# Kernel optimization log

Hardware: AMD Instinct MI355X
Metric: run time of the kernel (lower is better)

Reference implementation:

```python
import jax, jax.numpy as jnp
from jax import lax
import numpy as np
import math

INPUT_DIM = 64
HIDDEN_DIM = 512
SEQ_LEN = 256
BATCH = 512
PRED_LEN = 24
NUM_TARGETS = 1


def setup_inputs() -> dict:
    key = jax.random.key(0)
    ks = jax.random.split(key, 10)
    stdv = 1.0 / math.sqrt(HIDDEN_DIM)
    u = lambda k, shape: jax.random.uniform(k, shape, jnp.float32, -stdv, stdv)
    return {
        "x": jax.random.normal(ks[0], (BATCH, SEQ_LEN, INPUT_DIM), jnp.float32),
        "Wa": u(ks[1], (INPUT_DIM, INPUT_DIM)),
        "Ua": u(ks[2], (2 * HIDDEN_DIM, INPUT_DIM)),
        "ba": jnp.zeros((INPUT_DIM,), jnp.float32),
        "Va": u(ks[3], (INPUT_DIM, INPUT_DIM)),
        "W_ih": u(ks[4], (4 * HIDDEN_DIM, INPUT_DIM)),
        "W_hh": u(ks[5], (4 * HIDDEN_DIM, HIDDEN_DIM)),
        "b_ih": u(ks[6], (4 * HIDDEN_DIM,)),
        "b_hh": u(ks[7], (4 * HIDDEN_DIM,)),
        "fc_w": u(ks[8], (PRED_LEN * NUM_TARGETS, HIDDEN_DIM)),
        "fc_b": u(ks[9], (PRED_LEN * NUM_TARGETS,)),
    }


def reference(x, Wa, Ua, ba, Va, W_ih, W_hh, b_ih, b_hh, fc_w, fc_b):
    B, S, D = x.shape
    H = W_hh.shape[1]

    def step(carry, x_t):
        h, c = carry  # [B,H] each
        # attention gate over input features
        hc = jnp.concatenate([h, c], axis=1)  # [B,2H]
        a_t = jnp.tanh(x_t @ Wa + hc @ Ua + ba) @ Va  # [B,D]
        alpha_t = jax.nn.softmax(a_t, axis=1)
        x_att = alpha_t * x_t
        # torch.nn.LSTMCell: gates in order i, f, g, o
        gates = x_att @ W_ih.T + h @ W_hh.T + b_ih + b_hh  # [B,4H]
        i, f, g, o = jnp.split(gates, 4, axis=1)
        c_new = jax.nn.sigmoid(f) * c + jax.nn.sigmoid(i) * jnp.tanh(g)
        h_new = jax.nn.sigmoid(o) * jnp.tanh(c_new)
        return (h_new, c_new), None

    h0 = jnp.zeros((B, H), x.dtype)
    c0 = jnp.zeros((B, H), x.dtype)
    (h_T, _), _ = lax.scan(step, (h0, c0), jnp.swapaxes(x, 0, 1))  # scan over seq
    y = h_T @ fc_w.T + fc_b  # [B, pred_len*num_targets]
    return y.reshape(B, PRED_LEN, NUM_TARGETS)
```

## Files before the change

kernel.cpp:

```cpp
#include <hip/hip_runtime.h>
#include <math.h>

#define B 512
#define S 256
#define D 64
#define H 512
#define BH (B*H)


typedef __attribute__((ext_vector_type(8))) short short8;
typedef __attribute__((ext_vector_type(4))) float f32x4;

__device__ inline unsigned short f2bf(float v) {
    unsigned int u = __float_as_uint(v);
    unsigned int r = (u + 0x7fffu + ((u >> 16) & 1u)) >> 16;
    return (unsigned short)r;
}
__device__ inline float bf2f(unsigned short b) {
    return __uint_as_float(((unsigned int)b) << 16);
}

__global__ __launch_bounds__(256) void init_zero(
    float* __restrict__ h32, float* __restrict__ c32,
    unsigned short* __restrict__ hHi, unsigned short* __restrict__ hLo)
{
    int i = blockIdx.x * blockDim.x + threadIdx.x;
    if (i < BH) {
        h32[i] = 0.f;
        c32[i] = 0.f;
        hHi[i] = 0;
        hLo[i] = 0;
    }
}

__global__ __launch_bounds__(256) void prep_weights(
    const float* __restrict__ Whh, const float* __restrict__ Wih,
    unsigned short* __restrict__ wswz)
{
    const int ut = blockIdx.x;
    const int kb = blockIdx.y;
    const int t = threadIdx.x;
    const int srow = t >> 2;
    const int cc0 = (t & 3) * 16;
    const int Wrow = (srow & 3)*H + ut*16 + (srow >> 2);

    const float* src = (kb < 8) ? (Whh + (size_t)Wrow*H + kb*64 + cc0)
                                : (Wih + (size_t)Wrow*D + cc0);
    float v[16];
    #pragma unroll
    for (int i = 0; i < 4; ++i)
        *(float4*)&v[i*4] = *(const float4*)(src + i*4);

    unsigned short hi[16], lo[16];
    #pragma unroll
    for (int e = 0; e < 16; ++e) {
        hi[e] = f2bf(v[e]);
        lo[e] = f2bf(v[e] - bf2f(hi[e]));
    }
    #pragma unroll
    for (int g = 0; g < 2; ++g) {
        const int cc = cc0 + g*8;
        const int ks = cc >> 5;
        const int cg = (cc >> 3) & 3;
        size_t bh = ((((size_t)(ut*9 + kb)*2 + 0)*2 + ks)*64 + srow)*32 + cg*8;
        size_t bl = ((((size_t)(ut*9 + kb)*2 + 1)*2 + ks)*64 + srow)*32 + cg*8;
        *(short8*)(wswz + bh) = *(const short8*)&hi[g*8];
        *(short8*)(wswz + bl) = *(const short8*)&lo[g*8];
    }
}

__global__ __launch_bounds__(256) void attn_kernel(
    const float* __restrict__ x, const float* __restrict__ Wa,
    const float* __restrict__ Ua, const float* __restrict__ ba,
    const float* __restrict__ Va,
    const float* __restrict__ h32, const float* __restrict__ c32,
    unsigned short* __restrict__ xHi, unsigned short* __restrict__ xLo, int t)
{
    const int d = threadIdx.x & 63;
    const int r = (threadIdx.x >> 6) & 1;
    const int p = threadIdx.x >> 7;
    const int b = blockIdx.x * 2 + r;

    const int rd = t & 1;
    const float* __restrict__ hrow = h32 + (size_t)rd*BH + (size_t)b*H;
    const float* __restrict__ crow = c32 + (size_t)b*H;
    const float* __restrict__ xrow = x + ((size_t)b*S + t)*D;

    __shared__ float part[2][2][64];
    __shared__ float ta[2][64];
    __shared__ float pv[2][2][64];

    float a = 0.f;
    if (p == 0) {
        a = ba[d];
        #pragma unroll 8
        for (int k = 0; k < D; ++k) a += xrow[k] * Wa[k*D + d];
        #pragma unroll 8
        for (int k = 0; k < H; ++k) a += hrow[k] * Ua[k*D + d];
    } else {
        #pragma unroll 8
        for (int k = 0; k < H; ++k) a += crow[k] * Ua[(size_t)(H + k)*D + d];
    }
    part[r][p][d] = a;
    __syncthreads();
    if (p == 0) {
        ta[r][d] = tanhf(part[r][0][d] + part[r][1][d]);
    }
    __syncthreads();
    float av = 0.f;
    {
        const int k0 = p * 32;
        #pragma unroll 8
        for (int k = k0; k < k0 + 32; ++k) av += ta[r][k] * Va[k*D + d];
    }
    pv[r][p][d] = av;
    __syncthreads();
    float v = pv[r][0][d] + pv[r][1][d];
    float m = v;
    #pragma unroll
    for (int o = 32; o > 0; o >>= 1) m = fmaxf(m, __shfl_xor(m, o));
    float e = expf(v - m);
    float ssum = e;
    #pragma unroll
    for (int o = 32; o > 0; o >>= 1) ssum += __shfl_xor(ssum, o);
    if (p == 0) {
        float val = (e / ssum) * xrow[d];
        unsigned short hi = f2bf(val);
        unsigned short lo = f2bf(val - bf2f(hi));
        xHi[(size_t)b*D + d] = hi;
        xLo[(size_t)b*D + d] = lo;
    }
}

__global__ __launch_bounds__(256) void gates_kernel(
    const unsigned short* __restrict__ wswz,
    const unsigned short* __restrict__ hHi, const unsigned short* __restrict__ hLo,
    const unsigned short* __restrict__ xHi, const unsigned short* __restrict__ xLo,
    float* __restrict__ h32, float* __restrict__ c32,
    const float* __restrict__ bih, const float* __restrict__ bhh, int t)
{
    const int tid = threadIdx.x;
    const int lane = tid & 63;
    const int wid = tid >> 6;
    const int wr = wid >> 1, wc = wid & 1;
    const int ut = blockIdx.x;
    const int rt = blockIdx.y;
    const int b0 = rt * 64;
    const int u_base = ut * 16;
    const int l15 = lane & 15;
    const int cg = lane >> 4;

    __shared__ __align__(16) unsigned short aHi[2][64][72];
    __shared__ __align__(16) unsigned short aLo[2][64][72];
    __shared__ float gout[64][66];

    const int rd = t & 1, wrs = rd ^ 1;
    const unsigned short* __restrict__ hHiR = hHi + (size_t)rd*BH;
    const unsigned short* __restrict__ hLoR = hLo + (size_t)rd*BH;

    f32x4 acc00 = {0,0,0,0}, acc01 = {0,0,0,0}, acc10 = {0,0,0,0}, acc11 = {0,0,0,0};
    short8 bre[2][2][2][2];

    const int srow = tid >> 2;
    const int q4 = tid & 3;

    auto stageA = [&](int kb, int buf) {
        const unsigned short *sh, *sl;
        if (kb < 8) {
            size_t base = (size_t)(b0 + srow)*H + kb*64 + q4*16;
            sh = hHiR + base; sl = hLoR + base;
        } else {
            size_t base = (size_t)(b0 + srow)*D + q4*16;
            sh = xHi + base; sl = xLo + base;
        }
        *(short8*)&aHi[buf][srow][q4*16]     = *(const short8*)sh;
        *(short8*)&aHi[buf][srow][q4*16 + 8] = *(const short8*)(sh + 8);
        *(short8*)&aLo[buf][srow][q4*16]     = *(const short8*)sl;
        *(short8*)&aLo[buf][srow][q4*16 + 8] = *(const short8*)(sl + 8);
    };
    auto loadB = [&](int kb, int set) {
        #pragma unroll
        for (int half = 0; half < 2; ++half)
            #pragma unroll
            for (int ks = 0; ks < 2; ++ks)
                #pragma unroll
                for (int rb = 0; rb < 2; ++rb) {
                    const unsigned short* p = wswz +
                        ((((size_t)(ut*9 + kb)*2 + half)*2 + ks)*64
                         + wc*32 + rb*16 + l15)*32 + cg*8;
                    bre[set][half][ks][rb] = *(const short8*)p;
                }
    };

    stageA(0, 0);
    loadB(0, 0);
    __syncthreads();

    #pragma unroll
    for (int kb = 0; kb < 9; ++kb) {
        const int cur = kb & 1;
        if (kb < 8) {
            stageA(kb + 1, cur ^ 1);
            loadB(kb + 1, cur ^ 1);
        }
        #pragma unroll
        for (int ks = 0; ks < 2; ++ks) {
            const int col = ks*32 + cg*8;
            short8 ah0 = *(const short8*)&aHi[cur][wr*32 + l15][col];
            short8 ah1 = *(const short8*)&aHi[cur][wr*32 + 16 + l15][col];
            short8 al0 = *(const short8*)&aLo[cur][wr*32 + l15][col];
            short8 al1 = *(const short8*)&aLo[cur][wr*32 + 16 + l15][col];
            short8 bh0 = bre[cur][0][ks][0];
            short8 bh1 = bre[cur][0][ks][1];
            short8 bl0 = bre[cur][1][ks][0];
            short8 bl1 = bre[cur][1][ks][1];
            acc00 = __builtin_amdgcn_mfma_f32_16x16x32_bf16(ah0, bh0, acc00, 0,0,0);
            acc01 = __builtin_amdgcn_mfma_f32_16x16x32_bf16(ah0, bh1, acc01, 0,0,0);
            acc10 = __builtin_amdgcn_mfma_f32_16x16x32_bf16(ah1, bh0, acc10, 0,0,0);
            acc11 = __builtin_amdgcn_mfma_f32_16x16x32_bf16(ah1, bh1, acc11, 0,0,0);
            acc00 = __builtin_amdgcn_mfma_f32_16x16x32_bf16(ah0, bl0, acc00, 0,0,0);
            acc01 = __builtin_amdgcn_mfma_f32_16x16x32_bf16(ah0, bl1, acc01, 0,0,0);
            acc10 = __builtin_amdgcn_mfma_f32_16x16x32_bf16(ah1, bl0, acc10, 0,0,0);
            acc11 = __builtin_amdgcn_mfma_f32_16x16x32_bf16(ah1, bl1, acc11, 0,0,0);
            acc00 = __builtin_amdgcn_mfma_f32_16x16x32_bf16(al0, bh0, acc00, 0,0,0);
            acc01 = __builtin_amdgcn_mfma_f32_16x16x32_bf16(al0, bh1, acc01, 0,0,0);
            acc10 = __builtin_amdgcn_mfma_f32_16x16x32_bf16(al1, bh0, acc10, 0,0,0);
            acc11 = __builtin_amdgcn_mfma_f32_16x16x32_bf16(al1, bh1, acc11, 0,0,0);
        }
        __syncthreads();
    }

    {
        const int m0 = (lane >> 4) * 4;
        const int n0 = lane & 15;
        #pragma unroll
        for (int r = 0; r < 4; ++r) {
            gout[wr*32 + m0 + r     ][wc*32 + n0     ] = acc00[r];
            gout[wr*32 + m0 + r     ][wc*32 + 16 + n0] = acc01[r];
            gout[wr*32 + 16 + m0 + r][wc*32 + n0     ] = acc10[r];
            gout[wr*32 + 16 + m0 + r][wc*32 + 16 + n0] = acc11[r];
        }
    }
    __syncthreads();
    {
        const int u16 = tid & 15;
        const int u_glob = u_base + u16;
        const float bs0 = bih[0*H + u_glob] + bhh[0*H + u_glob];
        const float bs1 = bih[1*H + u_glob] + bhh[1*H + u_glob];
        const float bs2 = bih[2*H + u_glob] + bhh[2*H + u_glob];
        const float bs3 = bih[3*H + u_glob] + bhh[3*H + u_glob];
        float* __restrict__ h32w = h32 + (size_t)wrs*BH;
        unsigned short* __restrict__ hHiW = (unsigned short*)hHi + (size_t)wrs*BH;
        unsigned short* __restrict__ hLoW = (unsigned short*)hLo + (size_t)wrs*BH;
        #pragma unroll
        for (int pass = 0; pass < 4; ++pass) {
            const int b_loc = (tid >> 4) + pass*16;
            const int b = b0 + b_loc;
            float2 g01 = *(const float2*)&gout[b_loc][u16*4];
            float2 g23 = *(const float2*)&gout[b_loc][u16*4 + 2];
            float gi = g01.x + bs0;
            float gf = g01.y + bs1;
            float gg = g23.x + bs2;
            float go = g23.y + bs3;
            const size_t idx = (size_t)b*H + u_glob;
            float c_old = c32[idx];
            float si = 1.f/(1.f + expf(-gi));
            float sf = 1.f/(1.f + expf(-gf));
            float so = 1.f/(1.f + expf(-go));
            float cn = sf*c_old + si*tanhf(gg);
            float hn = so*tanhf(cn);
            c32[idx] = cn;
            h32w[idx] = hn;
            unsigned short hi = f2bf(hn);
            unsigned short lo = f2bf(hn - bf2f(hi));
            hHiW[idx] = hi;
            hLoW[idx] = lo;
        }
    }
}

__global__ __launch_bounds__(256) void fc_kernel(
    const float* __restrict__ fcw, const float* __restrict__ fcb,
    const float* __restrict__ h32, float* __restrict__ out)
{
    const int b = blockIdx.x;
    __shared__ float hrow[H];
    const float* __restrict__ hp = h32 + (size_t)b*H;
    for (int k = threadIdx.x; k < H; k += 256) hrow[k] = hp[k];
    __syncthreads();
    int j = threadIdx.x;
    if (j < 24) {
        float a = fcb[j];
        #pragma unroll 8
        for (int k = 0; k < H; ++k) a += hrow[k] * fcw[j*H + k];
        out[b*24 + j] = a;
    }
}

extern "C" void kernel_launch(void* const* d_in, const int* in_sizes, int n_in,
                              void* d_out, int out_size, void* d_ws, size_t ws_size,
                              hipStream_t stream) {
    const float* x   = (const float*)d_in[0];
    const float* Wa  = (const float*)d_in[1];
    const float* Ua  = (const float*)d_in[2];
    const float* ba  = (const float*)d_in[3];
    const float* Va  = (const float*)d_in[4];
    const float* Wih = (const float*)d_in[5];
    const float* Whh = (const float*)d_in[6];
    const float* bih = (const float*)d_in[7];
    const float* bhh = (const float*)d_in[8];
    const float* fcw = (const float*)d_in[9];
    const float* fcb = (const float*)d_in[10];
    float* out = (float*)d_out;

    char* base = (char*)d_ws;
    float* h32 = (float*)(base);
    float* c32 = (float*)(base + (size_t)2*BH*4);
    unsigned short* hHi = (unsigned short*)(base + (size_t)3*BH*4);
    unsigned short* hLo = hHi + (size_t)2*BH;
    unsigned short* xHi = hLo + (size_t)2*BH;
    unsigned short* xLo = xHi + (size_t)B*D;
    unsigned short* wswz = xLo + (size_t)B*D;

    hipLaunchKernelGGL(init_zero, dim3((BH + 255)/256), dim3(256), 0, stream,
                       h32, c32, hHi, hLo);
    hipLaunchKernelGGL(prep_weights, dim3(32, 9), dim3(256), 0, stream,
                       Whh, Wih, wswz);
    for (int t = 0; t < S; ++t) {
        hipLaunchKernelGGL(attn_kernel, dim3(B/2), dim3(256), 0, stream,
                           x, Wa, Ua, ba, Va, h32, c32, xHi, xLo, t);
        hipLaunchKernelGGL(gates_kernel, dim3(32, 8), dim3(256), 0, stream,
                           wswz, hHi, hLo, xHi, xLo, h32, c32, bih, bhh, t);
    }
    hipLaunchKernelGGL(fc_kernel, dim3(B), dim3(256), 0, stream, fcw, fcb, h32, out);
}
```

Baseline: 8.384 ms.

## Halve gate-column tile per block to double grid size in gates kernel

The gates kernel now covers 8 hidden units (32 gate columns) per block instead of 16, so the grid grows from 256 to 512 blocks on the 256-CU device. The weight swizzle layout is rebuilt to match, B fragments are loaded directly per k-block instead of being double-buffered in registers, and launch bounds request 2 blocks per CU. This aims to fill more CUs on a latency-bound per-timestep GEMM. In exchange, each A tile of h is now staged from global memory by twice as many blocks, and weight loads are no longer prefetched.

```diff
diff --git a/kernel.cpp b/kernel.cpp
--- a/kernel.cpp
+++ b/kernel.cpp
@@ -6,7 +6,6 @@
 #define D 64
 #define H 512
 #define BH (B*H)
-
 
 typedef __attribute__((ext_vector_type(8))) short short8;
 typedef __attribute__((ext_vector_type(4))) float f32x4;
@@ -37,36 +36,33 @@
     const float* __restrict__ Whh, const float* __restrict__ Wih,
     unsigned short* __restrict__ wswz)
 {
-    const int ut = blockIdx.x;
+    const int jt = blockIdx.x;
     const int kb = blockIdx.y;
     const int t = threadIdx.x;
-    const int srow = t >> 2;
-    const int cc0 = (t & 3) * 16;
-    const int Wrow = (srow & 3)*H + ut*16 + (srow >> 2);
-
-    const float* src = (kb < 8) ? (Whh + (size_t)Wrow*H + kb*64 + cc0)
-                                : (Wih + (size_t)Wrow*D + cc0);
-    float v[16];
+    const int jj = t >> 3;
+    const int kk8 = t & 7;
+    const int jg = jt*32 + jj;
+    const int u = jg >> 2, q = jg & 3;
+    const int Wrow = q*H + u;
+
+    const float* src = (kb < 8) ? (Whh + (size_t)Wrow*H + kb*64 + kk8*8)
+                                : (Wih + (size_t)Wrow*D + kk8*8);
+    float v[8];
+    *(float4*)&v[0] = *(const float4*)(src);
+    *(float4*)&v[4] = *(const float4*)(src + 4);
+
+    unsigned short hi[8], lo[8];
     #pragma unroll
-    for (int i = 0; i < 4; ++i)
-        *(float4*)&v[i*4] = *(const float4*)(src + i*4);
-
-    unsigned short hi[16], lo[16];
-    #pragma unroll
-    for (int e = 0; e < 16; ++e) {
+    for (int e = 0; e < 8; ++e) {
         hi[e] = f2bf(v[e]);
         lo[e] = f2bf(v[e] - bf2f(hi[e]));
     }
-    #pragma unroll
-    for (int g = 0; g < 2; ++g) {
-        const int cc = cc0 + g*8;
-        const int ks = cc >> 5;
-        const int cg = (cc >> 3) & 3;
-        size_t bh = ((((size_t)(ut*9 + kb)*2 + 0)*2 + ks)*64 + srow)*32 + cg*8;
-        size_t bl = ((((size_t)(ut*9 + kb)*2 + 1)*2 + ks)*64 + srow)*32 + cg*8;
-        *(short8*)(wswz + bh) = *(const short8*)&hi[g*8];
-        *(short8*)(wswz + bl) = *(const short8*)&lo[g*8];
-    }
+    const int ks = kk8 >> 2, cg = kk8 & 3;
+    const size_t slab = (size_t)(jt*9 + kb) * 4096;
+    const size_t oH = slab + (size_t)(0*2048 + ks*1024 + cg*256 + jj*8);
+    const size_t oL = slab + (size_t)(1*2048 + ks*1024 + cg*256 + jj*8);
+    *(short8*)(wswz + oH) = *(const short8*)hi;
+    *(short8*)(wswz + oL) = *(const short8*)lo;
 }
 
 __global__ __launch_bounds__(256) void attn_kernel(
@@ -132,7 +128,7 @@
     }
 }
 
-__global__ __launch_bounds__(256) void gates_kernel(
+__global__ __launch_bounds__(256, 2) void gates_kernel(
     const unsigned short* __restrict__ wswz,
     const unsigned short* __restrict__ hHi, const unsigned short* __restrict__ hLo,
     const unsigned short* __restrict__ xHi, const unsigned short* __restrict__ xLo,
@@ -143,108 +139,92 @@
     const int lane = tid & 63;
     const int wid = tid >> 6;
     const int wr = wid >> 1, wc = wid & 1;
-    const int ut = blockIdx.x;
-    const int rt = blockIdx.y;
-    const int b0 = rt * 64;
-    const int u_base = ut * 16;
+    const int jt = blockIdx.x;
+    const int b0 = blockIdx.y * 64;
     const int l15 = lane & 15;
     const int cg = lane >> 4;
 
     __shared__ __align__(16) unsigned short aHi[2][64][72];
     __shared__ __align__(16) unsigned short aLo[2][64][72];
-    __shared__ float gout[64][66];
+    __shared__ float gout[64][37];
 
     const int rd = t & 1, wrs = rd ^ 1;
     const unsigned short* __restrict__ hHiR = hHi + (size_t)rd*BH;
     const unsigned short* __restrict__ hLoR = hLo + (size_t)rd*BH;
 
-    f32x4 acc00 = {0,0,0,0}, acc01 = {0,0,0,0}, acc10 = {0,0,0,0}, acc11 = {0,0,0,0};
-    short8 bre[2][2][2][2];
-
     const int srow = tid >> 2;
     const int q4 = tid & 3;
 
-    auto stageA = [&](int kb, int buf) {
-        const unsigned short *sh, *sl;
-        if (kb < 8) {
-            size_t base = (size_t)(b0 + srow)*H + kb*64 + q4*16;
-            sh = hHiR + base; sl = hLoR + base;
-        } else {
-            size_t base = (size_t)(b0 + srow)*D + q4*16;
-            sh = xHi + base; sl = xLo + base;
-        }
-        *(short8*)&aHi[buf][srow][q4*16]     = *(const short8*)sh;
-        *(short8*)&aHi[buf][srow][q4*16 + 8] = *(const short8*)(sh + 8);
-        *(short8*)&aLo[buf][srow][q4*16]     = *(const short8*)sl;
-        *(short8*)&aLo[buf][srow][q4*16 + 8] = *(const short8*)(sl + 8);
-    };
-    auto loadB = [&](int kb, int set) {
-        #pragma unroll
-        for (int half = 0; half < 2; ++half)
-            #pragma unroll
-            for (int ks = 0; ks < 2; ++ks)
-                #pragma unroll
-                for (int rb = 0; rb < 2; ++rb) {
-                    const unsigned short* p = wswz +
-                        ((((size_t)(ut*9 + kb)*2 + half)*2 + ks)*64
-                         + wc*32 + rb*16 + l15)*32 + cg*8;
-                    bre[set][half][ks][rb] = *(const short8*)p;
-                }
-    };
-
-    stageA(0, 0);
-    loadB(0, 0);
-    __syncthreads();
-
-    #pragma unroll
+    {
+        const size_t base = (size_t)(b0 + srow)*H + q4*16;
+        *(short8*)&aHi[0][srow][q4*16]     = *(const short8*)(hHiR + base);
+        *(short8*)&aHi[0][srow][q4*16 + 8] = *(const short8*)(hHiR + base + 8);
+        *(short8*)&aLo[0][srow][q4*16]     = *(const short8*)(hLoR + base);
+        *(short8*)&aLo[0][srow][q4*16 + 8] = *(const short8*)(hLoR + base + 8);
+    }
+    __syncthreads();
+
+    f32x4 acc0 = {0,0,0,0}, acc1 = {0,0,0,0};
+    const int lofs = cg*256 + (wc*16 + l15)*8;
+
     for (int kb = 0; kb < 9; ++kb) {
         const int cur = kb & 1;
+        const unsigned short* pB = wswz + (size_t)(jt*9 + kb)*4096;
+        short8 bh0 = *(const short8*)(pB + 0*2048 + 0*1024 + lofs);
+        short8 bh1 = *(const short8*)(pB + 0*2048 + 1*1024 + lofs);
+        short8 bl0 = *(const short8*)(pB + 1*2048 + 0*1024 + lofs);
+        short8 bl1 = *(const short8*)(pB + 1*2048 + 1*1024 + lofs);
         if (kb < 8) {
-            stageA(kb + 1, cur ^ 1);
-            loadB(kb + 1, cur ^ 1);
+            const unsigned short *sh, *sl;
+            if (kb + 1 < 8) {
+                const size_t base = (size_t)(b0 + srow)*H + (kb + 1)*64 + q4*16;
+                sh = hHiR + base; sl = hLoR + base;
+            } else {
+                const size_t base = (size_t)(b0 + srow)*D + q4*16;
+                sh = xHi + base; sl = xLo + base;
+            }
+            *(short8*)&aHi[cur^1][srow][q4*16]     = *(const short8*)sh;
+            *(short8*)&aHi[cur^1][srow][q4*16 + 8] = *(const short8*)(sh + 8);
+            *(short8*)&aLo[cur^1][srow][q4*16]     = *(const short8*)sl;
+            *(short8*)&aLo[cur^1][srow][q4*16 + 8] = *(const short8*)(sl + 8);
         }
-        #pragma unroll
-        for (int ks = 0; ks < 2; ++ks) {
-            const int col = ks*32 + cg*8;
-            short8 ah0 = *(const short8*)&aHi[cur][wr*32 + l15][col];
-            short8 ah1 = *(const short8*)&aHi[cur][wr*32 + 16 + l15][col];
-            short8 al0 = *(const short8*)&aLo[cur][wr*32 + l15][col];
-            short8 al1 = *(const short8*)&aLo[cur][wr*32 + 16 + l15][col];
-            short8 bh0 = bre[cur][0][ks][0];
-            short8 bh1 = bre[cur][0][ks][1];
-            short8 bl0 = bre[cur][1][ks][0];
-            short8 bl1 = bre[cur][1][ks][1];
-            acc00 = __builtin_amdgcn_mfma_f32_16x16x32_bf16(ah0, bh0, acc00, 0,0,0);
-            acc01 = __builtin_amdgcn_mfma_f32_16x16x32_bf16(ah0, bh1, acc01, 0,0,0);
-            acc10 = __builtin_amdgcn_mfma_f32_16x16x32_bf16(ah1, bh0, acc10, 0,0,0);
-            acc11 = __builtin_amdgcn_mfma_f32_16x16x32_bf16(ah1, bh1, acc11, 0,0,0);
-            acc00 = __builtin_amdgcn_mfma_f32_16x16x32_bf16(ah0, bl0, acc00, 0,0,0);
-            acc01 = __builtin_amdgcn_mfma_f32_16x16x32_bf16(ah0, bl1, acc01, 0,0,0);
-            acc10 = __builtin_amdgcn_mfma_f32_16x16x32_bf16(ah1, bl0, acc10, 0,0,0);
-            acc11 = __builtin_amdgcn_mfma_f32_16x16x32_bf16(ah1, bl1, acc11, 0,0,0);
-            acc00 = __builtin_amdgcn_mfma_f32_16x16x32_bf16(al0, bh0, acc00, 0,0,0);
-            acc01 = __builtin_amdgcn_mfma_f32_16x16x32_bf16(al0, bh1, acc01, 0,0,0);
-            acc10 = __builtin_amdgcn_mfma_f32_16x16x32_bf16(al1, bh0, acc10, 0,0,0);
-            acc11 = __builtin_amdgcn_mfma_f32_16x16x32_bf16(al1, bh1, acc11, 0,0,0);
-        }
+        const int ar = wr*32 + l15;
+        short8 ah00 = *(const short8*)&aHi[cur][ar     ][cg*8];
+        short8 ah01 = *(const short8*)&aHi[cur][ar     ][32 + cg*8];
+        short8 ah10 = *(const short8*)&aHi[cur][ar + 16][cg*8];
+        short8 ah11 = *(const short8*)&aHi[cur][ar + 16][32 + cg*8];
+        short8 al00 = *(const short8*)&aLo[cur][ar     ][cg*8];
+        short8 al01 = *(const short8*)&aLo[cur][ar     ][32 + cg*8];
+        short8 al10 = *(const short8*)&aLo[cur][ar + 16][cg*8];
+        short8 al11 = *(const short8*)&aLo[cur][ar + 16][32 + cg*8];
+
+        acc0 = __builtin_amdgcn_mfma_f32_16x16x32_bf16(ah00, bh0, acc0, 0,0,0);
+        acc1 = __builtin_amdgcn_mfma_f32_16x16x32_bf16(ah10, bh0, acc1, 0,0,0);
+        acc0 = __builtin_amdgcn_mfma_f32_16x16x32_bf16(ah00, bl0, acc0, 0,0,0);
+        acc1 = __builtin_amdgcn_mfma_f32_16x16x32_bf16(ah10, bl0, acc1, 0,0,0);
+        acc0 = __builtin_amdgcn_mfma_f32_16x16x32_bf16(al00, bh0, acc0, 0,0,0);
+        acc1 = __builtin_amdgcn_mfma_f32_16x16x32_bf16(al10, bh0, acc1, 0,0,0);
+        acc0 = __builtin_amdgcn_mfma_f32_16x16x32_bf16(ah01, bh1, acc0, 0,0,0);
+        acc1 = __builtin_amdgcn_mfma_f32_16x16x32_bf16(ah11, bh1, acc1, 0,0,0);
+        acc0 = __builtin_amdgcn_mfma_f32_16x16x32_bf16(ah01, bl1, acc0, 0,0,0);
+        acc1 = __builtin_amdgcn_mfma_f32_16x16x32_bf16(ah11, bl1, acc1, 0,0,0);
+        acc0 = __builtin_amdgcn_mfma_f32_16x16x32_bf16(al01, bh1, acc0, 0,0,0);
+        acc1 = __builtin_amdgcn_mfma_f32_16x16x32_bf16(al11, bh1, acc1, 0,0,0);
         __syncthreads();
     }
 
     {
-        const int m0 = (lane >> 4) * 4;
-        const int n0 = lane & 15;
+        const int m0 = cg * 4;
         #pragma unroll
         for (int r = 0; r < 4; ++r) {
-            gout[wr*32 + m0 + r     ][wc*32 + n0     ] = acc00[r];
-            gout[wr*32 + m0 + r     ][wc*32 + 16 + n0] = acc01[r];
-            gout[wr*32 + 16 + m0 + r][wc*32 + n0     ] = acc10[r];
-            gout[wr*32 + 16 + m0 + r][wc*32 + 16 + n0] = acc11[r];
+            gout[wr*32 + m0 + r     ][wc*16 + l15] = acc0[r];
+            gout[wr*32 + 16 + m0 + r][wc*16 + l15] = acc1[r];
         }
     }
     __syncthreads();
     {
-        const int u16 = tid & 15;
-        const int u_glob = u_base + u16;
+        const int u8 = tid & 7;
+        const int u_glob = jt*8 + u8;
         const float bs0 = bih[0*H + u_glob] + bhh[0*H + u_glob];
         const float bs1 = bih[1*H + u_glob] + bhh[1*H + u_glob];
         const float bs2 = bih[2*H + u_glob] + bhh[2*H + u_glob];
@@ -253,15 +233,13 @@
         unsigned short* __restrict__ hHiW = (unsigned short*)hHi + (size_t)wrs*BH;
         unsigned short* __restrict__ hLoW = (unsigned short*)hLo + (size_t)wrs*BH;
         #pragma unroll
-        for (int pass = 0; pass < 4; ++pass) {
-            const int b_loc = (tid >> 4) + pass*16;
-            const int b = b0 + b_loc;
-            float2 g01 = *(const float2*)&gout[b_loc][u16*4];
-            float2 g23 = *(const float2*)&gout[b_loc][u16*4 + 2];
-            float gi = g01.x + bs0;
-            float gf = g01.y + bs1;
-            float gg = g23.x + bs2;
-            float go = g23.y + bs3;
+        for (int pp = 0; pp < 2; ++pp) {
+            const int row_loc = (tid >> 3) + pp*32;
+            const int b = b0 + row_loc;
+            float gi = gout[row_loc][u8*4 + 0] + bs0;
+            float gf = gout[row_loc][u8*4 + 1] + bs1;
+            float gg = gout[row_loc][u8*4 + 2] + bs2;
+            float go = gout[row_loc][u8*4 + 3] + bs3;
             const size_t idx = (size_t)b*H + u_glob;
             float c_old = c32[idx];
             float si = 1.f/(1.f + expf(-gi));
@@ -324,12 +302,12 @@
 
     hipLaunchKernelGGL(init_zero, dim3((BH + 255)/256), dim3(256), 0, stream,
                        h32, c32, hHi, hLo);
-    hipLaunchKernelGGL(prep_weights, dim3(32, 9), dim3(256), 0, stream,
+    hipLaunchKernelGGL(prep_weights, dim3(64, 9), dim3(256), 0, stream,
                        Whh, Wih, wswz);
     for (int t = 0; t < S; ++t) {
         hipLaunchKernelGGL(attn_kernel, dim3(B/2), dim3(256), 0, stream,
                            x, Wa, Ua, ba, Va, h32, c32, xHi, xLo, t);
-        hipLaunchKernelGGL(gates_kernel, dim3(32, 8), dim3(256), 0, stream,
+        hipLaunchKernelGGL(gates_kernel, dim3(64, 8), dim3(256), 0, stream,
                            wswz, hHi, hLo, xHi, xLo, h32, c32, bih, bhh, t);
     }
     hipLaunchKernelGGL(fc_kernel, dim3(B), dim3(256), 0, stream, fcw, fcb, h32, out);
```

Result: no change. 8.449 ms (+0.8%).
